# Kernel optimization log

Hardware: AMD Instinct MI355X
Metric: run time of the kernel (lower is better)

## Reference

```python
import jax, jax.numpy as jnp
import numpy as np

B, S, D, H = 8, 1024, 1024, 16
HD = D // H
EPS = 1e-5

def layernorm(x, g, b):
    mu = jnp.mean(x, axis=-1, keepdims=True)
    var = jnp.mean(jnp.square(x - mu), axis=-1, keepdims=True)
    return (x - mu) * jax.lax.rsqrt(var + EPS) * g + b

def setup_inputs() -> dict:
    key = jax.random.key(0)
    ks = jax.random.split(key, 8)
    s = 0.02
    return {
        "x": jax.random.normal(ks[0], (B, S, D), jnp.float32),
        "mask": jnp.tril(jnp.ones((S, S), jnp.int32)),  # causal mask
        "ln1_g": jnp.ones((D,), jnp.float32),
        "ln1_b": jnp.zeros((D,), jnp.float32),
        "wqkv": jax.random.normal(ks[1], (D, 3 * D), jnp.float32) * s,
        "bqkv": jnp.zeros((3 * D,), jnp.float32),
        "wo": jax.random.normal(ks[2], (D, D), jnp.float32) * s,
        "bo": jnp.zeros((D,), jnp.float32),
        "ln2_g": jnp.ones((D,), jnp.float32),
        "ln2_b": jnp.zeros((D,), jnp.float32),
        "w1": jax.random.normal(ks[3], (D, 4 * D), jnp.float32) * s,
        "b1": jnp.zeros((4 * D,), jnp.float32),
        "w2": jax.random.normal(ks[4], (4 * D, D), jnp.float32) * s,
        "b2": jnp.zeros((D,), jnp.float32),
    }

def reference(x, mask, ln1_g, ln1_b, wqkv, bqkv, wo, bo, ln2_g, ln2_b, w1, b1, w2, b2):
    # --- pre-LN attention ---
    h = layernorm(x, ln1_g, ln1_b)
    qkv = h @ wqkv + bqkv                                  # [B,S,3D]
    qkv = qkv.reshape(B, S, 3, H, HD).transpose(2, 0, 3, 1, 4)
    q, k, v = qkv[0], qkv[1], qkv[2]                       # [B,H,S,HD]
    scores = jnp.einsum('bhqd,bhkd->bhqk', q, k) / jnp.sqrt(jnp.float32(HD))
    scores = jnp.where(mask == 0, -jnp.inf, scores)
    attn = jax.nn.softmax(scores, axis=-1)
    out = jnp.einsum('bhqk,bhkd->bhqd', attn, v)           # [B,H,S,HD]
    out = out.transpose(0, 2, 1, 3).reshape(B, S, D)
    x = x + (out @ wo + bo)
    # --- pre-LN MLP ---
    h = layernorm(x, ln2_g, ln2_b)
    h = jax.nn.gelu(h @ w1 + b1, approximate=False)
    x = x + (h @ w2 + b2)
    return x
```

## Files before the change

### kernel.cpp

```cpp
#include <hip/hip_runtime.h>


#define DEV static __device__ __forceinline__

typedef __attribute__((ext_vector_type(8))) __bf16 bf16x8;
typedef __attribute__((ext_vector_type(4))) float f32x4;

DEV ushort f2bf(float f) {
  union { float f; unsigned u; } c; c.f = f;
  unsigned r = (c.u + 0x7FFFu + ((c.u >> 16) & 1u)) >> 16;
  return (ushort)r;
}

DEV float geluf(float v) {
  return 0.5f * v * (1.0f + erff(v * 0.70710678118654752f));
}

DEV void gload16(const ushort* g, ushort* l) {
  __builtin_amdgcn_global_load_lds(
      (const __attribute__((address_space(1))) void*)g,
      (__attribute__((address_space(3))) void*)l, 16, 0, 0);
}

__global__ __launch_bounds__(256)
void ln_bf16_kernel(const float* __restrict__ x, const float* __restrict__ g,
                    const float* __restrict__ bb, ushort* __restrict__ out)
{
  const int row = blockIdx.x, tid = threadIdx.x;
  const float4 v = ((const float4*)x)[row * 256 + tid];
  float s = v.x + v.y + v.z + v.w;
  float sq = v.x * v.x + v.y * v.y + v.z * v.z + v.w * v.w;
#pragma unroll
  for (int off = 32; off >= 1; off >>= 1) {
    s += __shfl_xor(s, off, 64);
    sq += __shfl_xor(sq, off, 64);
  }
  __shared__ float ps[4], pq[4];
  if ((tid & 63) == 0) { ps[tid >> 6] = s; pq[tid >> 6] = sq; }
  __syncthreads();
  s = ps[0] + ps[1] + ps[2] + ps[3];
  sq = pq[0] + pq[1] + pq[2] + pq[3];
  const float mu = s * (1.0f / 1024.0f);
  const float rstd = rsqrtf(sq * (1.0f / 1024.0f) - mu * mu + 1e-5f);
  const float4 gv = ((const float4*)g)[tid];
  const float4 bv = ((const float4*)bb)[tid];
  ushort4 o;
  o.x = f2bf((v.x - mu) * rstd * gv.x + bv.x);
  o.y = f2bf((v.y - mu) * rstd * gv.y + bv.y);
  o.z = f2bf((v.z - mu) * rstd * gv.z + bv.z);
  o.w = f2bf((v.w - mu) * rstd * gv.w + bv.w);
  ((ushort4*)out)[row * 256 + tid] = o;
}

__global__ __launch_bounds__(256)
void tcvt_kernel(const float* __restrict__ in, ushort* __restrict__ out, int K, int N)
{
  __shared__ float tile[32][33];
  const int tx = threadIdx.x & 31, ty = threadIdx.x >> 5;
  const int n0 = blockIdx.x * 32, k0 = blockIdx.y * 32;
#pragma unroll
  for (int j = 0; j < 4; ++j)
    tile[ty + j * 8][tx] = in[(size_t)(k0 + ty + j * 8) * N + n0 + tx];
  __syncthreads();
#pragma unroll
  for (int j = 0; j < 4; ++j)
    out[(size_t)(n0 + ty + j * 8) * K + k0 + tx] = f2bf(tile[tx][ty + j * 8]);
}

__global__ __launch_bounds__(256)
void vtr_kernel(const ushort* __restrict__ qkv, ushort* __restrict__ VT)
{
  __shared__ ushort tile[64][72];
  const int tid = threadIdx.x;
  const int bh = blockIdx.x, sb = blockIdx.y;
  const int b = bh >> 4, h = bh & 15;
  const int s0 = sb * 64;
#pragma unroll
  for (int it = 0; it < 2; ++it) {
    const int idx = it * 256 + tid;
    const int r = idx >> 3, hc = (idx & 7) * 8;
    *(int4*)&tile[r][hc] =
        *(const int4*)(qkv + ((size_t)b * 1024 + s0 + r) * 3072 + 2048 + h * 64 + hc);
  }
  __syncthreads();
#pragma unroll
  for (int it = 0; it < 2; ++it) {
    const int idx = it * 256 + tid;
    const int hd = idx >> 3, sc = (idx & 7) * 8;
    union { int4 v; ushort u[8]; } o;
#pragma unroll
    for (int j = 0; j < 8; ++j) o.u[j] = tile[sc + j][hd];
    *(int4*)(VT + ((size_t)bh * 64 + hd) * 1024 + s0 + sc) = o.v;
  }
}

template<int EPI>
__global__ __launch_bounds__(256)
void gemm_bf16(const ushort* __restrict__ A, const ushort* __restrict__ Bt,
               const float* __restrict__ bias, const float* __restrict__ resid,
               void* __restrict__ outp, int M, int N, int K)
{
  __shared__ ushort Asl[128 * 64];
  __shared__ ushort Bsl[128 * 64];
  const int tid = threadIdx.x;
  const int lane = tid & 63, w = tid >> 6;
  const int wm = w >> 1, wn = w & 1;
  const int grp = lane >> 4, r16 = lane & 15;
  const int bm = blockIdx.y * 128, bn = blockIdx.x * 128;

  const int lrow = lane >> 3;
  const int uswz = ((lane & 7) ^ lrow) * 8;
  const ushort* pa = A  + (size_t)(bm + w * 32 + lrow) * K + uswz;
  const ushort* pb = Bt + (size_t)(bn + w * 32 + lrow) * K + uswz;

  f32x4 acc[4][4] = {};

  for (int k0 = 0; k0 < K; k0 += 64) {
    __syncthreads();
#pragma unroll
    for (int i = 0; i < 4; ++i) {
      gload16(pa + (size_t)(i * 8) * K + k0, &Asl[(w * 32 + i * 8) * 64]);
      gload16(pb + (size_t)(i * 8) * K + k0, &Bsl[(w * 32 + i * 8) * 64]);
    }
    __syncthreads();
#pragma unroll
    for (int ks = 0; ks < 2; ++ks) {
      bf16x8 af[4], bfr[4];
#pragma unroll
      for (int m = 0; m < 4; ++m) {
        const int r = wm * 64 + m * 16 + r16;
        af[m] = *(const bf16x8*)&Asl[r * 64 + ((ks * 4 + grp) ^ (r16 & 7)) * 8];
      }
#pragma unroll
      for (int n = 0; n < 4; ++n) {
        const int r = wn * 64 + n * 16 + r16;
        bfr[n] = *(const bf16x8*)&Bsl[r * 64 + ((ks * 4 + grp) ^ (r16 & 7)) * 8];
      }
#pragma unroll
      for (int m = 0; m < 4; ++m)
#pragma unroll
        for (int n = 0; n < 4; ++n)
          acc[m][n] = __builtin_amdgcn_mfma_f32_16x16x32_bf16(af[m], bfr[n], acc[m][n], 0, 0, 0);
    }
  }

#pragma unroll
  for (int n = 0; n < 4; ++n) {
    const int col = bn + wn * 64 + n * 16 + r16;
    const float bval = bias[col];
#pragma unroll
    for (int m = 0; m < 4; ++m) {
      const int row0 = bm + wm * 64 + m * 16 + grp * 4;
#pragma unroll
      for (int r = 0; r < 4; ++r) {
        const size_t idx = (size_t)(row0 + r) * N + col;
        float v = acc[m][n][r] + bval;
        if (EPI == 1) v = geluf(v);
        if (EPI == 2) ((float*)outp)[idx] = v + resid[idx];
        else          ((ushort*)outp)[idx] = f2bf(v);
      }
    }
  }
}

template<int EPI>
__global__ __launch_bounds__(512, 2)
void gemm256(const ushort* __restrict__ A, const ushort* __restrict__ Bt,
             const float* __restrict__ bias, void* __restrict__ outp,
             int M, int N, int K)
{
  extern __shared__ ushort sm[];
  const int tid = threadIdx.x;
  const int lane = tid & 63, w = tid >> 6;
  const int wm = w >> 2, wn = w & 3;
  const int grp = lane >> 4, r16 = lane & 15;
  const int bm = blockIdx.y * 256, bn = blockIdx.x * 256;

  const int lrow = lane >> 3;
  const int uswz = ((lane & 7) ^ lrow) * 8;
  const ushort* pa = A  + (size_t)(bm + w * 32 + lrow) * K + uswz;
  const ushort* pb = Bt + (size_t)(bn + w * 32 + lrow) * K + uswz;

  const int nt = K >> 6;
  f32x4 acc[8][4] = {};

#pragma unroll
  for (int i = 0; i < 4; ++i) {
    gload16(pa + (size_t)(i * 8) * K, &sm[(w * 32 + i * 8) * 64]);
    gload16(pb + (size_t)(i * 8) * K, &sm[16384 + (w * 32 + i * 8) * 64]);
  }
#pragma unroll
  for (int i = 0; i < 4; ++i) {
    gload16(pa + (size_t)(i * 8) * K + 64, &sm[32768 + (w * 32 + i * 8) * 64]);
    gload16(pb + (size_t)(i * 8) * K + 64, &sm[32768 + 16384 + (w * 32 + i * 8) * 64]);
  }

  for (int t = 0; t < nt; ++t) {
    if (t + 1 < nt) { asm volatile("s_waitcnt vmcnt(8)" ::: "memory"); }
    else            { asm volatile("s_waitcnt vmcnt(0)" ::: "memory"); }
    __builtin_amdgcn_s_barrier();
    __builtin_amdgcn_sched_barrier(0);
    const ushort* as = sm + (t & 1) * 32768;
    const ushort* bs = as + 16384;
#pragma unroll
    for (int ks = 0; ks < 2; ++ks) {
      bf16x8 af[8], bfr[4];
#pragma unroll
      for (int mf = 0; mf < 8; ++mf) {
        const int r = wm * 128 + mf * 16 + r16;
        af[mf] = *(const bf16x8*)&as[r * 64 + ((ks * 4 + grp) ^ (r16 & 7)) * 8];
      }
#pragma unroll
      for (int nf = 0; nf < 4; ++nf) {
        const int r = wn * 64 + nf * 16 + r16;
        bfr[nf] = *(const bf16x8*)&bs[r * 64 + ((ks * 4 + grp) ^ (r16 & 7)) * 8];
      }
      __builtin_amdgcn_s_setprio(1);
#pragma unroll
      for (int mf = 0; mf < 8; ++mf)
#pragma unroll
        for (int nf = 0; nf < 4; ++nf)
          acc[mf][nf] = __builtin_amdgcn_mfma_f32_16x16x32_bf16(af[mf], bfr[nf], acc[mf][nf], 0, 0, 0);
      __builtin_amdgcn_s_setprio(0);
    }
    asm volatile("s_waitcnt lgkmcnt(0)" ::: "memory");
    __builtin_amdgcn_sched_barrier(0);
    __builtin_amdgcn_s_barrier();
    __builtin_amdgcn_sched_barrier(0);
    if (t + 2 < nt) {
      const int k0 = (t + 2) * 64;
      ushort* za = sm + (t & 1) * 32768;
      ushort* zb = za + 16384;
#pragma unroll
      for (int i = 0; i < 4; ++i) {
        gload16(pa + (size_t)(i * 8) * K + k0, &za[(w * 32 + i * 8) * 64]);
        gload16(pb + (size_t)(i * 8) * K + k0, &zb[(w * 32 + i * 8) * 64]);
      }
    }
  }

#pragma unroll
  for (int nf = 0; nf < 4; ++nf) {
    const int col = bn + wn * 64 + nf * 16 + r16;
    const float bval = bias[col];
#pragma unroll
    for (int mf = 0; mf < 8; ++mf) {
      const int row0 = bm + wm * 128 + mf * 16 + grp * 4;
#pragma unroll
      for (int r = 0; r < 4; ++r) {
        const size_t idx = (size_t)(row0 + r) * N + col;
        float v = acc[mf][nf][r] + bval;
        if (EPI == 1) v = geluf(v);
        ((ushort*)outp)[idx] = f2bf(v);
      }
    }
  }
}

__global__ __launch_bounds__(256)
void attn_kernel(const ushort* __restrict__ qkv, const ushort* __restrict__ VT,
                 ushort* __restrict__ out)
{
  __shared__ ushort Ks[64 * 64];
  __shared__ ushort Vs[64 * 64];
  __shared__ ushort Ps[4][16][72];
  const int tid = threadIdx.x, lane = tid & 63, w = tid >> 6;
  const int grp = lane >> 4, r16 = lane & 15;
  const int qb = 15 - blockIdx.x;
  const int bh = blockIdx.y;
  const int b = bh >> 4, h = bh & 15;
  const size_t rowbase = (size_t)b * 1024;
  const int q0 = qb * 64 + w * 16;

  bf16x8 qf[2];
  {
    const ushort* qp = qkv + (rowbase + q0 + r16) * 3072 + h * 64;
    qf[0] = *(const bf16x8*)(qp + grp * 8);
    qf[1] = *(const bf16x8*)(qp + 32 + grp * 8);
  }

  const int lrow = lane >> 3;
  const int uswz = ((lane & 7) ^ lrow) * 8;
  const ushort* kstg = qkv + (rowbase + w * 16 + lrow) * 3072 + 1024 + h * 64 + uswz;
  const ushort* vstg = VT + ((size_t)bh * 64 + w * 16 + lrow) * 1024 + uswz;

  f32x4 o[4] = {};
  float mrow[4] = {-1e30f, -1e30f, -1e30f, -1e30f};
  float lsum[4] = {0.f, 0.f, 0.f, 0.f};

  for (int kb = 0; kb <= qb; ++kb) {
    __syncthreads();
#pragma unroll
    for (int i = 0; i < 2; ++i) {
      gload16(kstg + (size_t)(kb * 64 + i * 8) * 3072, &Ks[(w * 16 + i * 8) * 64]);
      gload16(vstg + (size_t)(i * 8) * 1024 + kb * 64, &Vs[(w * 16 + i * 8) * 64]);
    }
    __syncthreads();

    f32x4 s[4] = {};
#pragma unroll
    for (int t = 0; t < 4; ++t) {
      const int r = t * 16 + r16;
#pragma unroll
      for (int f = 0; f < 2; ++f) {
        const bf16x8 kf = *(const bf16x8*)&Ks[r * 64 + ((f * 4 + grp) ^ (r16 & 7)) * 8];
        s[t] = __builtin_amdgcn_mfma_f32_16x16x32_bf16(qf[f], kf, s[t], 0, 0, 0);
      }
    }
#pragma unroll
    for (int t = 0; t < 4; ++t)
#pragma unroll
      for (int r = 0; r < 4; ++r) {
        float v = s[t][r] * 0.125f;
        if (kb == qb && (t * 16 + r16) > (w * 16 + grp * 4 + r)) v = -1e30f;
        s[t][r] = v;
      }
    float fac[4];
#pragma unroll
    for (int r = 0; r < 4; ++r) {
      float mx = fmaxf(fmaxf(s[0][r], s[1][r]), fmaxf(s[2][r], s[3][r]));
#pragma unroll
      for (int msk = 1; msk < 16; msk <<= 1) mx = fmaxf(mx, __shfl_xor(mx, msk, 16));
      const float mn = fmaxf(mrow[r], mx);
      fac[r] = __expf(mrow[r] - mn);
      mrow[r] = mn;
      lsum[r] *= fac[r];
    }
#pragma unroll
    for (int t = 0; t < 4; ++t)
#pragma unroll
      for (int r = 0; r < 4; ++r) o[t][r] *= fac[r];
    float rsum[4] = {0.f, 0.f, 0.f, 0.f};
#pragma unroll
    for (int t = 0; t < 4; ++t)
#pragma unroll
      for (int r = 0; r < 4; ++r) {
        const float p = __expf(s[t][r] - mrow[r]);
        s[t][r] = p;
        rsum[r] += p;
      }
#pragma unroll
    for (int r = 0; r < 4; ++r) {
#pragma unroll
      for (int msk = 1; msk < 16; msk <<= 1) rsum[r] += __shfl_xor(rsum[r], msk, 16);
      lsum[r] += rsum[r];
    }
#pragma unroll
    for (int t = 0; t < 4; ++t)
#pragma unroll
      for (int r = 0; r < 4; ++r)
        Ps[w][grp * 4 + r][t * 16 + r16] = f2bf(s[t][r]);
    bf16x8 pf[2];
    pf[0] = *(const bf16x8*)&Ps[w][r16][grp * 8];
    pf[1] = *(const bf16x8*)&Ps[w][r16][32 + grp * 8];
#pragma unroll
    for (int t = 0; t < 4; ++t) {
      const int r = t * 16 + r16;
#pragma unroll
      for (int f = 0; f < 2; ++f) {
        const bf16x8 vf = *(const bf16x8*)&Vs[r * 64 + ((f * 4 + grp) ^ (r16 & 7)) * 8];
        o[t] = __builtin_amdgcn_mfma_f32_16x16x32_bf16(pf[f], vf, o[t], 0, 0, 0);
      }
    }
  }

  float inv[4];
#pragma unroll
  for (int r = 0; r < 4; ++r) inv[r] = 1.0f / lsum[r];
#pragma unroll
  for (int t = 0; t < 4; ++t)
#pragma unroll
    for (int r = 0; r < 4; ++r) {
      const int qrow = qb * 64 + w * 16 + grp * 4 + r;
      out[(rowbase + qrow) * 1024 + h * 64 + t * 16 + r16] = f2bf(o[t][r] * inv[r]);
    }
}

extern "C" void kernel_launch(void* const* d_in, const int* in_sizes, int n_in,
                              void* d_out, int out_size, void* d_ws, size_t ws_size,
                              hipStream_t stream) {
  (void)in_sizes; (void)n_in; (void)out_size; (void)ws_size;
  const float* x     = (const float*)d_in[0];
  const float* ln1_g = (const float*)d_in[2];
  const float* ln1_b = (const float*)d_in[3];
  const float* wqkv  = (const float*)d_in[4];
  const float* bqkv  = (const float*)d_in[5];
  const float* wo    = (const float*)d_in[6];
  const float* bo    = (const float*)d_in[7];
  const float* ln2_g = (const float*)d_in[8];
  const float* ln2_b = (const float*)d_in[9];
  const float* w1    = (const float*)d_in[10];
  const float* b1    = (const float*)d_in[11];
  const float* w2    = (const float*)d_in[12];
  const float* b2    = (const float*)d_in[13];
  float* out = (float*)d_out;
  char* ws = (char*)d_ws;

  ushort* wqkvT = (ushort*)(ws + 0);
  ushort* woT   = (ushort*)(ws + 6291456);
  ushort* w1T   = (ushort*)(ws + 8388608);
  ushort* w2T   = (ushort*)(ws + 16777216);
  ushort* R1    = (ushort*)(ws + 25165824);
  ushort* R2    = (ushort*)(ws + 41943040);
  ushort* VT    = (ushort*)(ws + 41943040 + 50331648);

  hipFuncSetAttribute(reinterpret_cast<const void*>(gemm256<0>),
                      hipFuncAttributeMaxDynamicSharedMemorySize, 131072);
  hipFuncSetAttribute(reinterpret_cast<const void*>(gemm256<1>),
                      hipFuncAttributeMaxDynamicSharedMemorySize, 131072);

  const dim3 blk(256);
  tcvt_kernel<<<dim3(3072 / 32, 1024 / 32), blk, 0, stream>>>(wqkv, wqkvT, 1024, 3072);
  tcvt_kernel<<<dim3(1024 / 32, 1024 / 32), blk, 0, stream>>>(wo, woT, 1024, 1024);
  tcvt_kernel<<<dim3(4096 / 32, 1024 / 32), blk, 0, stream>>>(w1, w1T, 1024, 4096);
  tcvt_kernel<<<dim3(1024 / 32, 4096 / 32), blk, 0, stream>>>(w2, w2T, 4096, 1024);

  ln_bf16_kernel<<<8192, blk, 0, stream>>>(x, ln1_g, ln1_b, R1);
  gemm256<0><<<dim3(3072 / 256, 8192 / 256), 512, 131072, stream>>>(R1, wqkvT, bqkv, R2, 8192, 3072, 1024);
  vtr_kernel<<<dim3(128, 16), blk, 0, stream>>>(R2, VT);
  attn_kernel<<<dim3(16, 128), blk, 0, stream>>>(R2, VT, R1);
  gemm_bf16<2><<<dim3(1024 / 128, 8192 / 128), blk, 0, stream>>>(R1, woT, bo, x, out, 8192, 1024, 1024);
  ln_bf16_kernel<<<8192, blk, 0, stream>>>(out, ln2_g, ln2_b, R1);
  gemm256<1><<<dim3(4096 / 256, 8192 / 256), 512, 131072, stream>>>(R1, w1T, b1, R2, 8192, 4096, 1024);
  gemm_bf16<2><<<dim3(1024 / 128, 8192 / 128), blk, 0, stream>>>(R2, w2T, b2, out, out, 8192, 1024, 4096);
}
```

Measured before the change: 578.3 us.

## Double-buffer K/V tiles in attention and simplify GEMM prefetch pipeline

In the attention kernel, K and V tiles are now double-buffered in LDS. The next key block is prefetched while the current one is processed, which drops one barrier per iteration and overlaps global loads with MFMA work, at the cost of twice the LDS for K/V. In the 256x256 GEMM, the two-tiles-ahead prefetch with hand-placed waitcnt, barriers and setprio is replaced by a simpler one-tile-ahead scheme guarded by __syncthreads. The occupancy hint is also expressed as amdgpu_waves_per_eu(2,2). The simpler GEMM pipeline keeps fewer loads in flight and its full barrier waits on all outstanding memory operations, which may expose more load latency.

Result: no change. 567.1 us (-1.9%).

```diff
diff --git a/kernel.cpp b/kernel.cpp
--- a/kernel.cpp
+++ b/kernel.cpp
@@ -164,7 +164,7 @@
 }
 
 template<int EPI>
-__global__ __launch_bounds__(512, 2)
+__global__ __launch_bounds__(512) __attribute__((amdgpu_waves_per_eu(2, 2)))
 void gemm256(const ushort* __restrict__ A, const ushort* __restrict__ Bt,
              const float* __restrict__ bias, void* __restrict__ outp,
              int M, int N, int K)
@@ -189,17 +189,18 @@
     gload16(pa + (size_t)(i * 8) * K, &sm[(w * 32 + i * 8) * 64]);
     gload16(pb + (size_t)(i * 8) * K, &sm[16384 + (w * 32 + i * 8) * 64]);
   }
-#pragma unroll
-  for (int i = 0; i < 4; ++i) {
-    gload16(pa + (size_t)(i * 8) * K + 64, &sm[32768 + (w * 32 + i * 8) * 64]);
-    gload16(pb + (size_t)(i * 8) * K + 64, &sm[32768 + 16384 + (w * 32 + i * 8) * 64]);
-  }
 
   for (int t = 0; t < nt; ++t) {
-    if (t + 1 < nt) { asm volatile("s_waitcnt vmcnt(8)" ::: "memory"); }
-    else            { asm volatile("s_waitcnt vmcnt(0)" ::: "memory"); }
-    __builtin_amdgcn_s_barrier();
-    __builtin_amdgcn_sched_barrier(0);
+    __syncthreads();
+    if (t + 1 < nt) {
+      const int k0 = (t + 1) * 64;
+      ushort* za = sm + ((t + 1) & 1) * 32768;
+#pragma unroll
+      for (int i = 0; i < 4; ++i) {
+        gload16(pa + (size_t)(i * 8) * K + k0, &za[(w * 32 + i * 8) * 64]);
+        gload16(pb + (size_t)(i * 8) * K + k0, &za[16384 + (w * 32 + i * 8) * 64]);
+      }
+    }
     const ushort* as = sm + (t & 1) * 32768;
     const ushort* bs = as + 16384;
 #pragma unroll
@@ -215,27 +216,11 @@
         const int r = wn * 64 + nf * 16 + r16;
         bfr[nf] = *(const bf16x8*)&bs[r * 64 + ((ks * 4 + grp) ^ (r16 & 7)) * 8];
       }
-      __builtin_amdgcn_s_setprio(1);
 #pragma unroll
       for (int mf = 0; mf < 8; ++mf)
 #pragma unroll
         for (int nf = 0; nf < 4; ++nf)
           acc[mf][nf] = __builtin_amdgcn_mfma_f32_16x16x32_bf16(af[mf], bfr[nf], acc[mf][nf], 0, 0, 0);
-      __builtin_amdgcn_s_setprio(0);
-    }
-    asm volatile("s_waitcnt lgkmcnt(0)" ::: "memory");
-    __builtin_amdgcn_sched_barrier(0);
-    __builtin_amdgcn_s_barrier();
-    __builtin_amdgcn_sched_barrier(0);
-    if (t + 2 < nt) {
-      const int k0 = (t + 2) * 64;
-      ushort* za = sm + (t & 1) * 32768;
-      ushort* zb = za + 16384;
-#pragma unroll
-      for (int i = 0; i < 4; ++i) {
-        gload16(pa + (size_t)(i * 8) * K + k0, &za[(w * 32 + i * 8) * 64]);
-        gload16(pb + (size_t)(i * 8) * K + k0, &zb[(w * 32 + i * 8) * 64]);
-      }
     }
   }
 
@@ -261,8 +246,8 @@
 void attn_kernel(const ushort* __restrict__ qkv, const ushort* __restrict__ VT,
                  ushort* __restrict__ out)
 {
-  __shared__ ushort Ks[64 * 64];
-  __shared__ ushort Vs[64 * 64];
+  __shared__ ushort Ks[2 * 64 * 64];
+  __shared__ ushort Vs[2 * 64 * 64];
   __shared__ ushort Ps[4][16][72];
   const int tid = threadIdx.x, lane = tid & 63, w = tid >> 6;
   const int grp = lane >> 4, r16 = lane & 15;
@@ -288,14 +273,24 @@
   float mrow[4] = {-1e30f, -1e30f, -1e30f, -1e30f};
   float lsum[4] = {0.f, 0.f, 0.f, 0.f};
 
+#pragma unroll
+  for (int i = 0; i < 2; ++i) {
+    gload16(kstg + (size_t)(i * 8) * 3072, &Ks[(w * 16 + i * 8) * 64]);
+    gload16(vstg + (size_t)(i * 8) * 1024, &Vs[(w * 16 + i * 8) * 64]);
+  }
+
   for (int kb = 0; kb <= qb; ++kb) {
     __syncthreads();
-#pragma unroll
-    for (int i = 0; i < 2; ++i) {
-      gload16(kstg + (size_t)(kb * 64 + i * 8) * 3072, &Ks[(w * 16 + i * 8) * 64]);
-      gload16(vstg + (size_t)(i * 8) * 1024 + kb * 64, &Vs[(w * 16 + i * 8) * 64]);
-    }
-    __syncthreads();
+    if (kb < qb) {
+      const int nb = (kb + 1) & 1;
+#pragma unroll
+      for (int i = 0; i < 2; ++i) {
+        gload16(kstg + (size_t)((kb + 1) * 64 + i * 8) * 3072, &Ks[nb * 4096 + (w * 16 + i * 8) * 64]);
+        gload16(vstg + (size_t)(i * 8) * 1024 + (kb + 1) * 64, &Vs[nb * 4096 + (w * 16 + i * 8) * 64]);
+      }
+    }
+    const ushort* Kb = Ks + (kb & 1) * 4096;
+    const ushort* Vb = Vs + (kb & 1) * 4096;
 
     f32x4 s[4] = {};
 #pragma unroll
@@ -303,7 +298,7 @@
       const int r = t * 16 + r16;
 #pragma unroll
       for (int f = 0; f < 2; ++f) {
-        const bf16x8 kf = *(const bf16x8*)&Ks[r * 64 + ((f * 4 + grp) ^ (r16 & 7)) * 8];
+        const bf16x8 kf = *(const bf16x8*)&Kb[r * 64 + ((f * 4 + grp) ^ (r16 & 7)) * 8];
         s[t] = __builtin_amdgcn_mfma_f32_16x16x32_bf16(qf[f], kf, s[t], 0, 0, 0);
       }
     }
@@ -358,7 +353,7 @@
       const int r = t * 16 + r16;
 #pragma unroll
       for (int f = 0; f < 2; ++f) {
-        const bf16x8 vf = *(const bf16x8*)&Vs[r * 64 + ((f * 4 + grp) ^ (r16 & 7)) * 8];
+        const bf16x8 vf = *(const bf16x8*)&Vb[r * 64 + ((f * 4 + grp) ^ (r16 & 7)) * 8];
         o[t] = __builtin_amdgcn_mfma_f32_16x16x32_bf16(pf[f], vf, o[t], 0, 0, 0);
       }
     }
```
